# Optimization experiments

Measured on AMD Instinct MI355X. Metric: run time of the kernel, lower is better.

Reference implementation:

```python
import jax, jax.numpy as jnp
import numpy as np

N = 50000
E = 1600000
D_IN = 128
D_OUT = 128
K_EIG = 4
N_AGG = 3
N_SCALE = 3
AVG_D_LOG = float(np.log(33.0))  # avg_d['log'] for avg degree 32
BN_EPS = 1e-5


def setup_inputs() -> dict:
    key = jax.random.key(0)
    ks = jax.random.split(key, 8)
    h = jax.random.normal(ks[0], (N, D_IN), dtype=jnp.float32)
    eig = jax.random.normal(ks[1], (N, K_EIG), dtype=jnp.float32)
    snorm_n = jax.random.uniform(ks[2], (N, 1), dtype=jnp.float32)
    edge_src = jax.random.randint(ks[3], (E,), 0, N, dtype=jnp.int32)
    edge_dst = jax.random.randint(ks[4], (E,), 0, N, dtype=jnp.int32)
    d_cat = N_AGG * N_SCALE * D_IN  # 1152
    W = jax.random.normal(ks[5], (d_cat, D_OUT), dtype=jnp.float32) / np.sqrt(d_cat)
    b = jnp.zeros((D_OUT,), dtype=jnp.float32)
    bn_gamma = jnp.ones((D_OUT,), dtype=jnp.float32)
    bn_beta = jnp.zeros((D_OUT,), dtype=jnp.float32)
    bn_mean = jax.random.normal(ks[6], (D_OUT,), dtype=jnp.float32) * 0.1
    bn_var = jnp.ones((D_OUT,), dtype=jnp.float32)
    return {"h": h, "eig": eig, "snorm_n": snorm_n, "W": W, "b": b,
            "bn_gamma": bn_gamma, "bn_beta": bn_beta, "bn_mean": bn_mean,
            "bn_var": bn_var, "edge_src": edge_src, "edge_dst": edge_dst}


def reference(h, eig, snorm_n, W, b, bn_gamma, bn_beta, bn_mean, bn_var, edge_src, edge_dst):
    h_in = h
    # --- pretrans_edges: message e = src h; vector_field = eig_src - eig_dst ---
    h_e = h[edge_src]                      # [E, d] gathered edge messages
    vf = eig[edge_src] - eig[edge_dst]     # [E, k_eig]
    w = jnp.abs(vf[:, 0:1])                # dir1 weights [E, 1]

    # --- reduce: multi-aggregator segment reduce over destination nodes ---
    deg = jax.ops.segment_sum(jnp.ones((E,), h.dtype), edge_dst, num_segments=N)  # [N]
    deg_safe = jnp.maximum(deg, 1.0)
    sum_h = jax.ops.segment_sum(h_e, edge_dst, num_segments=N)
    mean_h = sum_h / deg_safe[:, None]
    max_h = jax.ops.segment_max(h_e, edge_dst, num_segments=N)
    max_h = jnp.where(deg[:, None] > 0, max_h, 0.0)  # empty mailbox -> 0
    dir_num = jax.ops.segment_sum(h_e * w, edge_dst, num_segments=N)
    dir_den = jax.ops.segment_sum(w, edge_dst, num_segments=N)  # [N, 1]
    dir_av = dir_num / (dir_den + 1e-30)
    agg = jnp.concatenate([mean_h, max_h, dir_av], axis=1)  # [N, 3d]

    # --- scalers: identity, amplification, attenuation ---
    logD = jnp.log(deg + 1.0)[:, None]
    amp = agg * (logD / AVG_D_LOG)
    att = agg * (AVG_D_LOG / jnp.maximum(logD, 1e-6))
    hcat = jnp.concatenate([agg, amp, att], axis=1)  # [N, 9d]

    # --- posttrans MLP (1 layer, no activation) ---
    out = hcat @ W + b
    # graph norm
    out = out * snorm_n
    # batch norm (eval mode, running stats)
    out = (out - bn_mean) * jax.lax.rsqrt(bn_var + BN_EPS) * bn_gamma + bn_beta
    out = jax.nn.relu(out)
    # residual (in_dim == out_dim)
    out = h_in + out
    # dropout p=0.0 / eval -> identity
    return out
```

## Files before the change

kernel.cpp:

```cpp
#include <hip/hip_runtime.h>
#include <hip/hip_bf16.h>

#define DIN 128
#define KEIG 4
#define BSH 7
#define BCAP 5120
#define ITEMS 16
#define AVG_D_LOG 3.4965075614664802f
#define BN_EPS 1e-5f

typedef __attribute__((ext_vector_type(8))) short bf16x8;
typedef __attribute__((ext_vector_type(4))) float f32x4;
typedef __attribute__((ext_vector_type(2))) float f32x2;

#define GLD16(SRC, DST) __builtin_amdgcn_global_load_lds(                     \
    (const __attribute__((address_space(1))) unsigned int*)(const void*)(SRC),\
    (__attribute__((address_space(3))) unsigned int*)(void*)(DST), 16, 0, 0)

static __device__ inline unsigned short f2bf(float f) {
    union { float f; unsigned u; } v; v.f = f;
    unsigned r = v.u + 0x7FFFu + ((v.u >> 16) & 1u);
    return (unsigned short)(r >> 16);
}
static __device__ inline unsigned pack2bf(float lo, float hi) {
    return (unsigned)f2bf(lo) | ((unsigned)f2bf(hi) << 16);
}
static __device__ inline f32x2 up2(unsigned u) {
    f32x2 r;
    r.x = __int_as_float(u << 16);
    r.y = __int_as_float(u & 0xffff0000u);
    return r;
}


__global__ void k_prep(const float* __restrict__ h, unsigned* __restrict__ hb,
                       const float* __restrict__ W, unsigned short* __restrict__ Wt,
                       const float* __restrict__ eig, float* __restrict__ eig0,
                       int* __restrict__ cursor, int* __restrict__ bcur,
                       int nPairs, int wTotal, int N, int nbk)
{
    int i = blockIdx.x * 256 + threadIdx.x;
    if (i < nPairs) {
        float2 v = reinterpret_cast<const float2*>(h)[i];
        hb[i] = pack2bf(v.x, v.y);
    }
    if (i < wTotal) {
        int k = i % 384;
        int rest = i / 384;
        int col = rest & 127;
        int s = rest >> 7;
        const int ks = k >> 5, kg = (k >> 3) & 3, ko = k & 7;
        const int c = s * 8 + kg * 2 + (col >> 6);
        const int lane = col & 63;
        const size_t idx = (size_t)ks * 12288 + c * 512 + lane * 8 + ko;
        Wt[idx] = f2bf(W[(s * 384 + k) * 128 + col]);
    }
    if (i < N) {
        eig0[i] = eig[(size_t)i * KEIG];
        cursor[i] = 0;
    }
    if (i < nbk) bcur[i] = 0;
}


__global__ void k_bucket(const int* __restrict__ src, const int* __restrict__ dst,
                         const float* __restrict__ eig0, int* __restrict__ bcur,
                         uint2* __restrict__ stag, int E, int nbk)
{
    __shared__ int lcnt[512];
    __shared__ int lbase[512];
    const int t = threadIdx.x;
    for (int b = t; b < nbk; b += 256) lcnt[b] = 0;
    __syncthreads();

    const int e0 = blockIdx.x * (256 * ITEMS);
    int   bky[ITEMS];
    int   rnk[ITEMS];
    uint2 rec[ITEMS];
#pragma unroll
    for (int k = 0; k < ITEMS; ++k) {
        const int e = e0 + t + k * 256;
        if (e < E) {
            const int s = src[e], d = dst[e];
            const float w = fabsf(eig0[s] - eig0[d]);
            rec[k] = make_uint2(((unsigned)f2bf(w) << 16) | (unsigned)s, (unsigned)d);
            bky[k] = d >> BSH;
            rnk[k] = atomicAdd(&lcnt[bky[k]], 1);
        } else bky[k] = -1;
    }
    __syncthreads();
    for (int b = t; b < nbk; b += 256) {
        const int c = lcnt[b];
        lbase[b] = c ? atomicAdd(&bcur[b], c) : 0;
    }
    __syncthreads();
#pragma unroll
    for (int k = 0; k < ITEMS; ++k) {
        if (bky[k] >= 0) {
            const int pos = lbase[bky[k]] + rnk[k];
            if (pos < BCAP) stag[(size_t)bky[k] * BCAP + pos] = rec[k];
        }
    }
}


__global__ void k_group(const int* __restrict__ bcur, const uint2* __restrict__ stag,
                        unsigned* __restrict__ final_, int2* __restrict__ offcnt, int N)
{
    __shared__ uint2 sst[BCAP];
    __shared__ int hcnt[128];
    __shared__ int sbuf[2][128];
    const int b = blockIdx.x;
    const int t = threadIdx.x;
    const int cb = min(bcur[b], BCAP);

    for (int i = t; i < cb; i += 256) sst[i] = stag[(size_t)b * BCAP + i];
    if (t < 128) hcnt[t] = 0;
    __syncthreads();

    int dl[(BCAP + 255) / 256];
    int rk[(BCAP + 255) / 256];
    int nit = 0;
    for (int i = t; i < cb; i += 256) {
        const int d_loc = sst[i].y & 127;
        dl[nit] = d_loc;
        rk[nit] = atomicAdd(&hcnt[d_loc], 1);
        ++nit;
    }
    __syncthreads();

    int cur = 0;
    if (t < 128) sbuf[0][t] = hcnt[t];
    __syncthreads();
    for (int d = 1; d < 128; d <<= 1) {
        if (t < 128) {
            int x = sbuf[cur][t];
            if (t >= d) x += sbuf[cur][t - d];
            sbuf[cur ^ 1][t] = x;
        }
        cur ^= 1;
        __syncthreads();
    }
    const int exb = cur ^ 1;
    if (t < 128) sbuf[exb][t] = sbuf[cur][t] - hcnt[t];
    __syncthreads();

    if (t < 128) {
        const int dg = (b << BSH) + t;
        if (dg < N) offcnt[dg] = make_int2(b * BCAP + sbuf[exb][t], hcnt[t]);
    }
    nit = 0;
    for (int i = t; i < cb; i += 256) {
        final_[(size_t)b * BCAP + sbuf[exb][dl[nit]] + rk[nit]] = sst[i].x;
        ++nit;
    }
}


__global__ void k_hist(const int* __restrict__ dst, int* __restrict__ counts, int E) {
    int e = blockIdx.x * 256 + threadIdx.x;
    if (e < E) atomicAdd(&counts[dst[e]], 1);
}

__global__ void k_part(const int* __restrict__ counts, int* __restrict__ part, int N) {
    __shared__ int red[4];
    const int t = threadIdx.x;
    const int i = blockIdx.x * 256 + t;
    int v = (i < N) ? counts[i] : 0;
    for (int d = 32; d >= 1; d >>= 1) v += __shfl_down(v, d, 64);
    if ((t & 63) == 0) red[t >> 6] = v;
    __syncthreads();
    if (t == 0) part[blockIdx.x] = red[0] + red[1] + red[2] + red[3];
}

__global__ void k_scan1(const int* __restrict__ part, int* __restrict__ partoff,
                        int* __restrict__ total_out, int NB) {
    __shared__ int buf[2][256];
    const int t = threadIdx.x;
    int v = (t < NB) ? part[t] : 0;
    buf[0][t] = v;
    __syncthreads();
    int cur = 0;
    for (int d = 1; d < 256; d <<= 1) {
        int x = buf[cur][t];
        if (t >= d) x += buf[cur][t - d];
        buf[cur ^ 1][t] = x;
        cur ^= 1;
        __syncthreads();
    }
    if (t < NB) partoff[t] = buf[cur][t] - v;
    if (t == 255) *total_out = buf[cur][255];
}

__global__ void k_off(const int* __restrict__ counts, const int* __restrict__ partoff,
                      int* __restrict__ offsets, int* __restrict__ cursor, int N) {
    __shared__ int buf[2][256];
    const int t = threadIdx.x;
    const int i = blockIdx.x * 256 + t;
    int v = (i < N) ? counts[i] : 0;
    buf[0][t] = v;
    __syncthreads();
    int cur = 0;
    for (int d = 1; d < 256; d <<= 1) {
        int x = buf[cur][t];
        if (t >= d) x += buf[cur][t - d];
        buf[cur ^ 1][t] = x;
        cur ^= 1;
        __syncthreads();
    }
    if (i < N) {
        int excl = partoff[blockIdx.x] + buf[cur][t] - v;
        offsets[i] = excl;
        cursor[i]  = excl;
    }
}

__global__ void k_fill_csr(const int* __restrict__ src, const int* __restrict__ dst,
                           const float* __restrict__ eig0, int* __restrict__ cursor,
                           int2* __restrict__ sedge, int E)
{
    int e = blockIdx.x * 256 + threadIdx.x;
    if (e < E) {
        int s = src[e], d = dst[e];
        float w = fabsf(eig0[s] - eig0[d]);
        int pos = atomicAdd(&cursor[d], 1);
        sedge[pos] = make_int2(s, __float_as_int(w));
    }
}


template<bool PACKED>
__launch_bounds__(256, 4)
__global__ void k_agg(const unsigned* __restrict__ hb,
                      const int2* __restrict__ offcnt, const int* __restrict__ offsets,
                      const unsigned* __restrict__ upk, const int2* __restrict__ sedge,
                      unsigned short* __restrict__ agg, float2* __restrict__ scal, int N)
{
    const int tid = threadIdx.x;
    const int qid = tid >> 4;
    const int l16 = tid & 15;
    const int n = blockIdx.x * 16 + qid;
    if (n >= N) return;

    int e0, cnt;
    if (PACKED) { const int2 oc = offcnt[n]; e0 = oc.x; cnt = oc.y; }
    else        { e0 = offsets[n]; cnt = offsets[n + 1] - e0; }

    const uint4* __restrict__ hb4 = reinterpret_cast<const uint4*>(hb);

    f32x2 s2[4], m2[4], d2[4];
    float wsum = 0.f;
#pragma unroll
    for (int f = 0; f < 4; ++f) {
        s2[f] = (f32x2){0.f, 0.f};
        m2[f] = (f32x2){-INFINITY, -INFINITY};
        d2[f] = (f32x2){0.f, 0.f};
    }
    const int clampi = (cnt > 0) ? cnt - 1 : 0;

    uint4 bufA[8], bufB[8];
    float wvA[8], wvB[8];

#define STAGE(BUF, WV, BASE) do {                                        \
    _Pragma("unroll")                                                    \
    for (int j = 0; j < 8; ++j) {                                        \
        int ci = (BASE) + j; ci = ci < clampi ? ci : clampi;             \
        unsigned sidx;                                                   \
        if (PACKED) {                                                    \
            const unsigned u = upk[e0 + ci];                             \
            WV[j] = __int_as_float(u & 0xffff0000u);                     \
            sidx = (u & 0xffffu) << 4;                                   \
        } else {                                                         \
            const int2 v = sedge[e0 + ci];                               \
            WV[j] = __int_as_float(v.y);                                 \
            sidx = ((unsigned)v.x) << 4;                                 \
        }                                                                \
        BUF[j] = hb4[sidx | (unsigned)l16];                              \
    }                                                                    \
} while (0)

#define ACCUM(BUF, WV, BASE) do {                                        \
    _Pragma("unroll")                                                    \
    for (int j = 0; j < 8; ++j) {                                        \
        if ((BASE) + j < cnt) {                                          \
            const float wj = WV[j];                                      \
            const f32x2 wj2 = (f32x2){wj, wj};                           \
            const f32x2 p0 = up2(BUF[j].x), p1 = up2(BUF[j].y);          \
            const f32x2 p2 = up2(BUF[j].z), p3 = up2(BUF[j].w);          \
            s2[0] += p0; s2[1] += p1; s2[2] += p2; s2[3] += p3;          \
            m2[0].x = fmaxf(m2[0].x, p0.x); m2[0].y = fmaxf(m2[0].y, p0.y); \
            m2[1].x = fmaxf(m2[1].x, p1.x); m2[1].y = fmaxf(m2[1].y, p1.y); \
            m2[2].x = fmaxf(m2[2].x, p2.x); m2[2].y = fmaxf(m2[2].y, p2.y); \
            m2[3].x = fmaxf(m2[3].x, p3.x); m2[3].y = fmaxf(m2[3].y, p3.y); \
            d2[0] += p0 * wj2; d2[1] += p1 * wj2;                        \
            d2[2] += p2 * wj2; d2[3] += p3 * wj2;                        \
            wsum += wj;                                                  \
        }                                                                \
    }                                                                    \
} while (0)

    if (cnt > 0) {
        STAGE(bufA, wvA, 0);
        for (int base = 0; base < cnt; base += 16) {
            const bool haveB = (base + 8) < cnt;
            if (haveB) STAGE(bufB, wvB, base + 8);
            ACCUM(bufA, wvA, base);
            if (base + 16 < cnt) STAGE(bufA, wvA, base + 16);
            if (haveB) ACCUM(bufB, wvB, base + 8);
        }
    }
#undef STAGE
#undef ACCUM

    const float degf = (float)cnt;
    const float inv  = 1.0f / fmaxf(degf, 1.0f);
    const float dinv = 1.0f / (wsum + 1e-30f);
    const bool nz = (cnt > 0);
    uint4 pm, px, pd;
    pm.x = pack2bf(s2[0].x * inv, s2[0].y * inv);
    pm.y = pack2bf(s2[1].x * inv, s2[1].y * inv);
    pm.z = pack2bf(s2[2].x * inv, s2[2].y * inv);
    pm.w = pack2bf(s2[3].x * inv, s2[3].y * inv);
    px.x = pack2bf(nz ? m2[0].x : 0.f, nz ? m2[0].y : 0.f);
    px.y = pack2bf(nz ? m2[1].x : 0.f, nz ? m2[1].y : 0.f);
    px.z = pack2bf(nz ? m2[2].x : 0.f, nz ? m2[2].y : 0.f);
    px.w = pack2bf(nz ? m2[3].x : 0.f, nz ? m2[3].y : 0.f);
    pd.x = pack2bf(d2[0].x * dinv, d2[0].y * dinv);
    pd.y = pack2bf(d2[1].x * dinv, d2[1].y * dinv);
    pd.z = pack2bf(d2[2].x * dinv, d2[2].y * dinv);
    pd.w = pack2bf(d2[3].x * dinv, d2[3].y * dinv);

    uint4* aggv = reinterpret_cast<uint4*>(agg);
    const int mt = n >> 6, row = n & 63;
    const size_t b4 = (size_t)mt * 3072 + (size_t)(l16 & 3) * 64 + row;
    const int kshi = l16 >> 2;
    aggv[b4 + (size_t)(0 * 4 + kshi) * 256] = pm;
    aggv[b4 + (size_t)(1 * 4 + kshi) * 256] = px;
    aggv[b4 + (size_t)(2 * 4 + kshi) * 256] = pd;
    if (l16 == 0) {
        const float logD = logf(degf + 1.0f);
        scal[n] = make_float2(logD / AVG_D_LOG, AVG_D_LOG / fmaxf(logD, 1e-6f));
    }
}


__launch_bounds__(256, 2)
__global__ void k_mm(const unsigned short* __restrict__ agg, const float2* __restrict__ scal,
                     const float* __restrict__ h, const float* __restrict__ snorm,
                     const float* __restrict__ bvec, const float* __restrict__ gam,
                     const float* __restrict__ bet, const float* __restrict__ bmean,
                     const float* __restrict__ bvar, const unsigned short* __restrict__ Wt,
                     float* __restrict__ out, int N, int nT)
{
    __shared__ char smem[33792];
    unsigned short* As = (unsigned short*)smem;
    unsigned short* Bs = (unsigned short*)(smem + 8192);
    float* outS = (float*)smem;

    const int tid  = threadIdx.x;
    const int wave = tid >> 6;
    const int lane = tid & 63;
    const int r16  = lane & 15;
    const int kgrp = lane >> 4;
    const int cb = wave * 32;

    const int mt0 = blockIdx.x * 2;
    const int mt1 = (mt0 + 1 < nT) ? (mt0 + 1) : mt0;
    const char* aggb0 = (const char*)agg + (size_t)mt0 * 49152;
    const char* aggb1 = (const char*)agg + (size_t)mt1 * 49152;
    const char* wtbase = (const char*)Wt;

    auto stage = [&](int ks) {
        GLD16(aggb0 + (size_t)ks * 4096 + wave * 1024 + lane * 16,
              (char*)As + (size_t)wave * 1024);
        GLD16(aggb1 + (size_t)ks * 4096 + wave * 1024 + lane * 16,
              (char*)As + (size_t)(4 + wave) * 1024);
#pragma unroll
        for (int i = 0; i < 6; ++i) {
            const int c = wave * 6 + i;
            GLD16(wtbase + (size_t)ks * 24576 + (size_t)c * 1024 + lane * 16,
                  (char*)Bs + (size_t)c * 1024);
        }
    };

    f32x4 acc[2][4][2][3];
#pragma unroll
    for (int t = 0; t < 2; ++t)
#pragma unroll
        for (int m = 0; m < 4; ++m)
#pragma unroll
            for (int ct = 0; ct < 2; ++ct)
#pragma unroll
                for (int sv = 0; sv < 3; ++sv)
                    acc[t][m][ct][sv] = (f32x4){0.f, 0.f, 0.f, 0.f};

    for (int ks = 0; ks < 12; ++ks) {
        if (ks) __syncthreads();
        stage(ks);
        __syncthreads();

        bf16x8 a0[4], a1[4], b[6];
#pragma unroll
        for (int m = 0; m < 4; ++m) {
            a0[m] = *reinterpret_cast<const bf16x8*>(
                &As[((size_t)kgrp * 64 + m * 16 + r16) * 8]);
            a1[m] = *reinterpret_cast<const bf16x8*>(
                &As[((size_t)(4 + kgrp) * 64 + m * 16 + r16) * 8]);
        }
#pragma unroll
        for (int sv = 0; sv < 3; ++sv)
#pragma unroll
            for (int ct = 0; ct < 2; ++ct)
                b[sv * 2 + ct] = *reinterpret_cast<const bf16x8*>(
                    &Bs[(((size_t)sv * 4 + kgrp) * 128 + cb + ct * 16 + r16) * 8]);
#pragma unroll
        for (int sv = 0; sv < 3; ++sv)
#pragma unroll
            for (int ct = 0; ct < 2; ++ct)
#pragma unroll
                for (int m = 0; m < 4; ++m) {
                    acc[0][m][ct][sv] = __builtin_amdgcn_mfma_f32_16x16x32_bf16(
                        a0[m], b[sv * 2 + ct], acc[0][m][ct][sv], 0, 0, 0);
                    acc[1][m][ct][sv] = __builtin_amdgcn_mfma_f32_16x16x32_bf16(
                        a1[m], b[sv * 2 + ct], acc[1][m][ct][sv], 0, 0, 0);
                }
    }

    __syncthreads();
#pragma unroll
    for (int t = 0; t < 2; ++t) {
        if (t == 1 && mt1 == mt0) break;
        const int nb = (t ? mt1 : mt0) * 64;
#pragma unroll
        for (int ct = 0; ct < 2; ++ct) {
            const int col = cb + ct * 16 + r16;
            const float bc  = bvec[col];
            const float mc  = bmean[col];
            const float rs  = rsqrtf(bvar[col] + BN_EPS);
            const float gc  = gam[col];
            const float bec = bet[col];
#pragma unroll
            for (int m = 0; m < 4; ++m) {
#pragma unroll
                for (int r = 0; r < 4; ++r) {
                    const int row = m * 16 + kgrp * 4 + r;
                    const int n  = nb + row;
                    float sn = 0.f; float2 sc = make_float2(0.f, 0.f);
                    if (n < N) { sn = snorm[n]; sc = scal[n]; }
                    float v = acc[t][m][ct][0][r] + sc.x * acc[t][m][ct][1][r]
                                                  + sc.y * acc[t][m][ct][2][r];
                    float y = (v + bc) * sn;
                    y = (y - mc) * rs * gc + bec;
                    y = fmaxf(y, 0.f);
                    outS[row * 132 + col] = y;
                }
            }
        }
        __syncthreads();
        const int rows = (N - nb < 64) ? (N - nb) : 64;
#pragma unroll
        for (int it = 0; it < 8; ++it) {
            const int idx = it * 256 + tid;
            const int row = idx >> 5;
            const int c4  = idx & 31;
            if (row < rows) {
                const float4 hv = *reinterpret_cast<const float4*>(
                    &h[(size_t)(nb + row) * 128 + c4 * 4]);
                float4 yv = *reinterpret_cast<const float4*>(&outS[row * 132 + c4 * 4]);
                yv.x += hv.x; yv.y += hv.y; yv.z += hv.z; yv.w += hv.w;
                *reinterpret_cast<float4*>(&out[(size_t)(nb + row) * 128 + c4 * 4]) = yv;
            }
        }
        __syncthreads();
    }
}


extern "C" void kernel_launch(void* const* d_in, const int* in_sizes, int n_in,
                              void* d_out, int out_size, void* d_ws, size_t ws_size,
                              hipStream_t stream)
{
    const float* h     = (const float*)d_in[0];
    const float* eig   = (const float*)d_in[1];
    const float* snorm = (const float*)d_in[2];
    const float* W     = (const float*)d_in[3];
    const float* bvec  = (const float*)d_in[4];
    const float* gam   = (const float*)d_in[5];
    const float* bet   = (const float*)d_in[6];
    const float* bmean = (const float*)d_in[7];
    const float* bvar  = (const float*)d_in[8];
    const int*   esrc  = (const int*)d_in[9];
    const int*   edst  = (const int*)d_in[10];
    float* out = (float*)d_out;

    const int N = in_sizes[0] / DIN;
    const int E = in_sizes[9];
    const int NB = (N + 255) / 256;
    const int nPairs = N * DIN / 2;
    const int wTotal = 3 * 128 * 384;
    const int nbk = (N + 127) >> BSH;
    const int N64 = (N + 63) / 64;
    const int N128 = (N + 127) / 128;
    (void)ws_size; (void)n_in; (void)out_size;

    char* base = (char*)d_ws;
    size_t o = 0;
    auto take = [&](size_t bytes) {
        char* p = base + o;
        o = (o + bytes + 255) & ~(size_t)255;
        return p;
    };
    unsigned* hb       = (unsigned*)take((size_t)nPairs * 4);
    unsigned short* Wt = (unsigned short*)take((size_t)wTotal * 2);
    float* eig0        = (float*)take((size_t)N * 4);
    int* cursor        = (int*)take((size_t)(N + 1) * 4);
    float2* scal       = (float2*)take((size_t)N * 8);

    const size_t agg_bytes  = (size_t)N64 * 49152;
    const size_t stag_bytes = (size_t)nbk * BCAP * 8;
    const size_t shared_bytes = agg_bytes > stag_bytes ? agg_bytes : stag_bytes;

    const size_t bucket_bytes = (size_t)nbk * BCAP * 4
                              + (size_t)N * 8
                              + (size_t)nbk * 4
                              + shared_bytes + 8192;
    const bool bucketOK = (N <= 65536) && (nbk <= 512) && ((o + bucket_bytes) <= ws_size);

    const int gridPrep = (nPairs + 255) / 256;
    const int gridE    = (E + 255) / 256;
    const int gridB    = (E + 256 * ITEMS - 1) / (256 * ITEMS);
    const int gridN16  = (N + 15) / 16;

    if (bucketOK) {
        unsigned* fin   = (unsigned*)take((size_t)nbk * BCAP * 4);
        int2* offcnt    = (int2*)take((size_t)N * 8);
        int* bcur       = (int*)take((size_t)nbk * 4);
        char* shared    = take(shared_bytes);
        uint2* stag     = (uint2*)shared;
        unsigned short* agg = (unsigned short*)shared;

        k_prep<<<gridPrep, 256, 0, stream>>>(h, hb, W, Wt, eig, eig0, cursor, bcur,
                                             nPairs, wTotal, N, nbk);
        k_bucket<<<gridB, 256, 0, stream>>>(esrc, edst, eig0, bcur, stag, E, nbk);
        k_group<<<nbk, 256, 0, stream>>>(bcur, stag, fin, offcnt, N);
        k_agg<true><<<gridN16, 256, 0, stream>>>(hb, offcnt, nullptr, fin, nullptr,
                                                 agg, scal, N);
        k_mm<<<N128, 256, 0, stream>>>(agg, scal, h, snorm, bvec, gam, bet, bmean, bvar,
                                       Wt, out, N, N64);
    } else {
        int* counts  = (int*)take((size_t)(N + 1) * 4);
        int* offsets = (int*)take((size_t)(N + 1) * 4);
        int2* sedge  = (int2*)take((size_t)(E + 16) * 8);
        int* part    = (int*)take((size_t)NB * 4);
        int* partoff = (int*)take((size_t)NB * 4);
        int* bcur    = (int*)take(4096);
        unsigned short* agg = (unsigned short*)take(agg_bytes);

        k_prep<<<gridPrep, 256, 0, stream>>>(h, hb, W, Wt, eig, eig0, counts, bcur,
                                             nPairs, wTotal, N, 1);
        k_hist<<<gridE, 256, 0, stream>>>(edst, counts, E);
        k_part<<<NB, 256, 0, stream>>>(counts, part, N);
        k_scan1<<<1, 256, 0, stream>>>(part, partoff, &offsets[N], NB);
        k_off<<<NB, 256, 0, stream>>>(counts, partoff, offsets, cursor, N);
        k_fill_csr<<<gridE, 256, 0, stream>>>(esrc, edst, eig0, cursor, sedge, E);
        k_agg<false><<<gridN16, 256, 0, stream>>>(hb, nullptr, offsets, nullptr, sedge,
                                                  agg, scal, N);
        k_mm<<<N128, 256, 0, stream>>>(agg, scal, h, snorm, bvec, gam, bet, bmean, bvar,
                                       Wt, out, N, N64);
    }
}
```

Before: 150.6 us.

## Fuse prep with edge bucketing and double-buffer the MFMA GEMM stages

Merges the bf16 conversion of h and W with the edge-bucketing pass into one launch. Bucket blocks now read eig directly instead of a precomputed eig0 array, and the bucket counters are cleared with a memset. In k_mm, LDS staging becomes double-buffered so the next K-slice's global-to-LDS loads are issued before computing on the current one, dropping one barrier per iteration. The price is LDS growing to 64KB per block, which may cut occupancy below the launch_bounds target of 2 blocks per CU. There is also a memset launch and strided eig reads in the bucket path.

```diff
diff --git a/kernel.cpp b/kernel.cpp
--- a/kernel.cpp
+++ b/kernel.cpp
@@ -30,6 +30,123 @@
     r.x = __int_as_float(u << 16);
     r.y = __int_as_float(u & 0xffff0000u);
     return r;
+}
+
+
+__global__ void k_pb(const float* __restrict__ h, unsigned* __restrict__ hb,
+                     const float* __restrict__ W, unsigned short* __restrict__ Wt,
+                     const float* __restrict__ eig,
+                     const int* __restrict__ src, const int* __restrict__ dst,
+                     int* __restrict__ bcur, uint2* __restrict__ stag,
+                     int nPairs, int wTotal, int E, int nbk, int gridB)
+{
+    __shared__ int lcnt[512];
+    __shared__ int lbase[512];
+    const int t = threadIdx.x;
+
+    if ((int)blockIdx.x < gridB) {
+        for (int b = t; b < nbk; b += 256) lcnt[b] = 0;
+        __syncthreads();
+
+        const int e0 = blockIdx.x * (256 * ITEMS);
+        int   bky[ITEMS];
+        int   rnk[ITEMS];
+        uint2 rec[ITEMS];
+#pragma unroll
+        for (int k = 0; k < ITEMS; ++k) {
+            const int e = e0 + t + k * 256;
+            if (e < E) {
+                const int s = src[e], d = dst[e];
+                const float w = fabsf(eig[(size_t)s * KEIG] - eig[(size_t)d * KEIG]);
+                rec[k] = make_uint2(((unsigned)f2bf(w) << 16) | (unsigned)s, (unsigned)d);
+                bky[k] = d >> BSH;
+                rnk[k] = atomicAdd(&lcnt[bky[k]], 1);
+            } else bky[k] = -1;
+        }
+        __syncthreads();
+        for (int b = t; b < nbk; b += 256) {
+            const int c = lcnt[b];
+            lbase[b] = c ? atomicAdd(&bcur[b], c) : 0;
+        }
+        __syncthreads();
+#pragma unroll
+        for (int k = 0; k < ITEMS; ++k) {
+            if (bky[k] >= 0) {
+                const int pos = lbase[bky[k]] + rnk[k];
+                if (pos < BCAP) stag[(size_t)bky[k] * BCAP + pos] = rec[k];
+            }
+        }
+    } else {
+        const int i = ((int)blockIdx.x - gridB) * 256 + t;
+        if (i < nPairs) {
+            float2 v = reinterpret_cast<const float2*>(h)[i];
+            hb[i] = pack2bf(v.x, v.y);
+        }
+        if (i < wTotal) {
+            int k = i % 384;
+            int rest = i / 384;
+            int col = rest & 127;
+            int s = rest >> 7;
+            const int ks = k >> 5, kg = (k >> 3) & 3, ko = k & 7;
+            const int c = s * 8 + kg * 2 + (col >> 6);
+            const int lane = col & 63;
+            const size_t idx = (size_t)ks * 12288 + c * 512 + lane * 8 + ko;
+            Wt[idx] = f2bf(W[(s * 384 + k) * 128 + col]);
+        }
+    }
+}
+
+
+__global__ void k_group(const int* __restrict__ bcur, const uint2* __restrict__ stag,
+                        unsigned* __restrict__ final_, int2* __restrict__ offcnt, int N)
+{
+    __shared__ uint2 sst[BCAP];
+    __shared__ int hcnt[128];
+    __shared__ int sbuf[2][128];
+    const int b = blockIdx.x;
+    const int t = threadIdx.x;
+    const int cb = min(bcur[b], BCAP);
+
+    for (int i = t; i < cb; i += 256) sst[i] = stag[(size_t)b * BCAP + i];
+    if (t < 128) hcnt[t] = 0;
+    __syncthreads();
+
+    int dl[(BCAP + 255) / 256];
+    int rk[(BCAP + 255) / 256];
+    int nit = 0;
+    for (int i = t; i < cb; i += 256) {
+        const int d_loc = sst[i].y & 127;
+        dl[nit] = d_loc;
+        rk[nit] = atomicAdd(&hcnt[d_loc], 1);
+        ++nit;
+    }
+    __syncthreads();
+
+    int cur = 0;
+    if (t < 128) sbuf[0][t] = hcnt[t];
+    __syncthreads();
+    for (int d = 1; d < 128; d <<= 1) {
+        if (t < 128) {
+            int x = sbuf[cur][t];
+            if (t >= d) x += sbuf[cur][t - d];
+            sbuf[cur ^ 1][t] = x;
+        }
+        cur ^= 1;
+        __syncthreads();
+    }
+    const int exb = cur ^ 1;
+    if (t < 128) sbuf[exb][t] = sbuf[cur][t] - hcnt[t];
+    __syncthreads();
+
+    if (t < 128) {
+        const int dg = (b << BSH) + t;
+        if (dg < N) offcnt[dg] = make_int2(b * BCAP + sbuf[exb][t], hcnt[t]);
+    }
+    nit = 0;
+    for (int i = t; i < cb; i += 256) {
+        final_[(size_t)b * BCAP + sbuf[exb][dl[nit]] + rk[nit]] = sst[i].x;
+        ++nit;
+    }
 }
 
 
@@ -61,101 +178,6 @@
     }
     if (i < nbk) bcur[i] = 0;
 }
-
-
-__global__ void k_bucket(const int* __restrict__ src, const int* __restrict__ dst,
-                         const float* __restrict__ eig0, int* __restrict__ bcur,
-                         uint2* __restrict__ stag, int E, int nbk)
-{
-    __shared__ int lcnt[512];
-    __shared__ int lbase[512];
-    const int t = threadIdx.x;
-    for (int b = t; b < nbk; b += 256) lcnt[b] = 0;
-    __syncthreads();
-
-    const int e0 = blockIdx.x * (256 * ITEMS);
-    int   bky[ITEMS];
-    int   rnk[ITEMS];
-    uint2 rec[ITEMS];
-#pragma unroll
-    for (int k = 0; k < ITEMS; ++k) {
-        const int e = e0 + t + k * 256;
-        if (e < E) {
-            const int s = src[e], d = dst[e];
-            const float w = fabsf(eig0[s] - eig0[d]);
-            rec[k] = make_uint2(((unsigned)f2bf(w) << 16) | (unsigned)s, (unsigned)d);
-            bky[k] = d >> BSH;
-            rnk[k] = atomicAdd(&lcnt[bky[k]], 1);
-        } else bky[k] = -1;
-    }
-    __syncthreads();
-    for (int b = t; b < nbk; b += 256) {
-        const int c = lcnt[b];
-        lbase[b] = c ? atomicAdd(&bcur[b], c) : 0;
-    }
-    __syncthreads();
-#pragma unroll
-    for (int k = 0; k < ITEMS; ++k) {
-        if (bky[k] >= 0) {
-            const int pos = lbase[bky[k]] + rnk[k];
-            if (pos < BCAP) stag[(size_t)bky[k] * BCAP + pos] = rec[k];
-        }
-    }
-}
-
-
-__global__ void k_group(const int* __restrict__ bcur, const uint2* __restrict__ stag,
-                        unsigned* __restrict__ final_, int2* __restrict__ offcnt, int N)
-{
-    __shared__ uint2 sst[BCAP];
-    __shared__ int hcnt[128];
-    __shared__ int sbuf[2][128];
-    const int b = blockIdx.x;
-    const int t = threadIdx.x;
-    const int cb = min(bcur[b], BCAP);
-
-    for (int i = t; i < cb; i += 256) sst[i] = stag[(size_t)b * BCAP + i];
-    if (t < 128) hcnt[t] = 0;
-    __syncthreads();
-
-    int dl[(BCAP + 255) / 256];
-    int rk[(BCAP + 255) / 256];
-    int nit = 0;
-    for (int i = t; i < cb; i += 256) {
-        const int d_loc = sst[i].y & 127;
-        dl[nit] = d_loc;
-        rk[nit] = atomicAdd(&hcnt[d_loc], 1);
-        ++nit;
-    }
-    __syncthreads();
-
-    int cur = 0;
-    if (t < 128) sbuf[0][t] = hcnt[t];
-    __syncthreads();
-    for (int d = 1; d < 128; d <<= 1) {
-        if (t < 128) {
-            int x = sbuf[cur][t];
-            if (t >= d) x += sbuf[cur][t - d];
-            sbuf[cur ^ 1][t] = x;
-        }
-        cur ^= 1;
-        __syncthreads();
-    }
-    const int exb = cur ^ 1;
-    if (t < 128) sbuf[exb][t] = sbuf[cur][t] - hcnt[t];
-    __syncthreads();
-
-    if (t < 128) {
-        const int dg = (b << BSH) + t;
-        if (dg < N) offcnt[dg] = make_int2(b * BCAP + sbuf[exb][t], hcnt[t]);
-    }
-    nit = 0;
-    for (int i = t; i < cb; i += 256) {
-        final_[(size_t)b * BCAP + sbuf[exb][dl[nit]] + rk[nit]] = sst[i].x;
-        ++nit;
-    }
-}
-
 
 __global__ void k_hist(const int* __restrict__ dst, int* __restrict__ counts, int E) {
     int e = blockIdx.x * 256 + threadIdx.x;
@@ -352,9 +374,9 @@
                      const float* __restrict__ bvar, const unsigned short* __restrict__ Wt,
                      float* __restrict__ out, int N, int nT)
 {
-    __shared__ char smem[33792];
-    unsigned short* As = (unsigned short*)smem;
-    unsigned short* Bs = (unsigned short*)(smem + 8192);
+    __shared__ char smem[65536];
+    char* AsB = smem;
+    char* BsB = smem + 16384;
     float* outS = (float*)smem;
 
     const int tid  = threadIdx.x;
@@ -370,16 +392,16 @@
     const char* aggb1 = (const char*)agg + (size_t)mt1 * 49152;
     const char* wtbase = (const char*)Wt;
 
-    auto stage = [&](int ks) {
+    auto stage = [&](int ks, int bf) {
         GLD16(aggb0 + (size_t)ks * 4096 + wave * 1024 + lane * 16,
-              (char*)As + (size_t)wave * 1024);
+              AsB + (size_t)bf * 8192 + wave * 1024);
         GLD16(aggb1 + (size_t)ks * 4096 + wave * 1024 + lane * 16,
-              (char*)As + (size_t)(4 + wave) * 1024);
+              AsB + (size_t)bf * 8192 + 4096 + wave * 1024);
 #pragma unroll
         for (int i = 0; i < 6; ++i) {
             const int c = wave * 6 + i;
             GLD16(wtbase + (size_t)ks * 24576 + (size_t)c * 1024 + lane * 16,
-                  (char*)Bs + (size_t)c * 1024);
+                  BsB + (size_t)bf * 24576 + (size_t)c * 1024);
         }
     };
 
@@ -394,25 +416,27 @@
                 for (int sv = 0; sv < 3; ++sv)
                     acc[t][m][ct][sv] = (f32x4){0.f, 0.f, 0.f, 0.f};
 
+    stage(0, 0);
     for (int ks = 0; ks < 12; ++ks) {
-        if (ks) __syncthreads();
-        stage(ks);
-        __syncthreads();
+        const int bf = ks & 1;
+        __syncthreads();
+        if (ks + 1 < 12) stage(ks + 1, bf ^ 1);
 
         bf16x8 a0[4], a1[4], b[6];
 #pragma unroll
         for (int m = 0; m < 4; ++m) {
             a0[m] = *reinterpret_cast<const bf16x8*>(
-                &As[((size_t)kgrp * 64 + m * 16 + r16) * 8]);
+                AsB + (size_t)bf * 8192 + ((size_t)kgrp * 64 + m * 16 + r16) * 16);
             a1[m] = *reinterpret_cast<const bf16x8*>(
-                &As[((size_t)(4 + kgrp) * 64 + m * 16 + r16) * 8]);
+                AsB + (size_t)bf * 8192 + 4096 + ((size_t)kgrp * 64 + m * 16 + r16) * 16);
         }
 #pragma unroll
         for (int sv = 0; sv < 3; ++sv)
 #pragma unroll
             for (int ct = 0; ct < 2; ++ct)
                 b[sv * 2 + ct] = *reinterpret_cast<const bf16x8*>(
-                    &Bs[(((size_t)sv * 4 + kgrp) * 128 + cb + ct * 16 + r16) * 8]);
+                    BsB + (size_t)bf * 24576 +
+                    (((size_t)sv * 4 + kgrp) * 128 + cb + ct * 16 + r16) * 16);
 #pragma unroll
         for (int sv = 0; sv < 3; ++sv)
 #pragma unroll
@@ -539,9 +563,10 @@
         uint2* stag     = (uint2*)shared;
         unsigned short* agg = (unsigned short*)shared;
 
-        k_prep<<<gridPrep, 256, 0, stream>>>(h, hb, W, Wt, eig, eig0, cursor, bcur,
-                                             nPairs, wTotal, N, nbk);
-        k_bucket<<<gridB, 256, 0, stream>>>(esrc, edst, eig0, bcur, stag, E, nbk);
+        hipMemsetAsync(bcur, 0, (size_t)nbk * 4, stream);
+        k_pb<<<gridB + gridPrep, 256, 0, stream>>>(h, hb, W, Wt, eig, esrc, edst,
+                                                   bcur, stag, nPairs, wTotal, E,
+                                                   nbk, gridB);
         k_group<<<nbk, 256, 0, stream>>>(bcur, stag, fin, offcnt, N);
         k_agg<true><<<gridN16, 256, 0, stream>>>(hb, offcnt, nullptr, fin, nullptr,
                                                  agg, scal, N);
```

Result: no change. 153.0 us (+1.6%).
